# Optimization experiments

Hardware: AMD Instinct MI355X
Metric: run time of the kernel (lower is better)

## Reference

```python
import jax, jax.numpy as jnp
import numpy as np

N = 20000
E = 320000
IN = 256
H = 4
C = 64
NEG_SLOPE = 0.2


def setup_inputs() -> dict:
    key = jax.random.key(0)
    ks = jax.random.split(key, 12)
    HC = H * C

    def w(k, shape, fan_in):
        return jax.random.normal(k, shape, dtype=jnp.float32) / np.sqrt(fan_in)

    x = jax.random.normal(ks[0], (N, IN), dtype=jnp.float32)
    edge_index = jax.random.randint(ks[1], (2, E), 0, N, dtype=jnp.int64)
    return {
        "x": x,
        "edge_index": edge_index,
        "Wl1": w(ks[2], (IN, HC), IN),
        "Wr1": w(ks[3], (IN, HC), IN),
        "att1": w(ks[4], (H, C), C),
        "b1": jnp.zeros((HC,), dtype=jnp.float32),
        "Wl2": w(ks[5], (HC, HC), HC),
        "Wr2": w(ks[6], (HC, HC), HC),
        "att2": w(ks[7], (H, C), C),
        "b2": jnp.zeros((HC,), dtype=jnp.float32),
        "Wfc": w(ks[8], (HC, 2), HC),
        "bfc": jnp.zeros((2,), dtype=jnp.float32),
    }


def _gatv2(x, src, dst, Wl, Wr, att, b):
    """GATv2Conv (concat=True, share_weights=False), inference (no dropout)."""
    n = x.shape[0]
    xl = (x @ Wl).reshape(n, H, C)  # source-side projection
    xr = (x @ Wr).reshape(n, H, C)  # target-side projection
    # per-edge GATv2 score: a^T LeakyReLU(xl_j + xr_i)
    e = jax.nn.leaky_relu(xl[src] + xr[dst], NEG_SLOPE)      # [E, H, C]
    score = jnp.einsum("ehc,hc->eh", e, att)                 # [E, H]
    # segment softmax over incoming edges of each target node
    smax = jax.ops.segment_max(score, dst, num_segments=n)   # [N, H]
    ex = jnp.exp(score - smax[dst])
    denom = jax.ops.segment_sum(ex, dst, num_segments=n)     # [N, H]
    alpha = ex / denom[dst]                                  # [E, H]
    # scatter-aggregate messages (source projections weighted by alpha)
    out = jax.ops.segment_sum(alpha[:, :, None] * xl[src], dst, num_segments=n)
    return out.reshape(n, H * C) + b


def reference(x, edge_index, Wl1, Wr1, att1, b1, Wl2, Wr2, att2, b2, Wfc, bfc):
    n = x.shape[0]
    # add_self_loops=True (PyG default)
    loop = jnp.arange(n, dtype=edge_index.dtype)
    src = jnp.concatenate([edge_index[0], loop])
    dst = jnp.concatenate([edge_index[1], loop])

    h = _gatv2(x, src, dst, Wl1, Wr1, att1, b1)
    h = jax.nn.relu(h)
    h = _gatv2(h, src, dst, Wl2, Wr2, att2, b2)
    h = jax.nn.relu(h)
    g = jnp.mean(h, axis=0, keepdims=True)  # [1, H*C]
    return g @ Wfc + bfc                    # [1, 2]
```

## Files before the change

### kernel.cpp

```cpp
#include <hip/hip_runtime.h>
#include <hip/hip_bf16.h>
#include <math.h>

#define Nn 20000
#define Ee 320000
#define INF_ 256
#define Hh 4
#define Cc 64
#define HC 256
#define NEG_SLOPE 0.2f

using frag16 = __attribute__((ext_vector_type(8))) short;
using f32x4  = __attribute__((ext_vector_type(4))) float;

__device__ __forceinline__ void async16(const void* g, void* l) {
    __builtin_amdgcn_global_load_lds(
        (const __attribute__((address_space(1))) unsigned int*)g,
        (__attribute__((address_space(3))) unsigned int*)l,
        16, 0, 0);
}


__global__ void init_deg(int* deg, int n) {
    int i = blockIdx.x * blockDim.x + threadIdx.x;
    if (i < n) deg[i] = 1;
}

__global__ void hist_kernel(const int* __restrict__ dst, int ne, int* deg) {
    int e = blockIdx.x * blockDim.x + threadIdx.x;
    if (e < ne) atomicAdd(&deg[dst[e]], 1);
}

__global__ __launch_bounds__(256) void scan1(const int* __restrict__ deg,
                                             int* __restrict__ excl,
                                             int* __restrict__ bsum, int n) {
    int tid = threadIdx.x;
    int gid = blockIdx.x * 256 + tid;
    int lane = tid & 63;
    int v = (gid < n) ? deg[gid] : 0;
    int x = v;
    #pragma unroll
    for (int off = 1; off < 64; off <<= 1) {
        int y = __shfl_up(x, off, 64);
        if (lane >= off) x += y;
    }
    __shared__ int wsum[4];
    if (lane == 63) wsum[tid >> 6] = x;
    __syncthreads();
    int wadd = 0;
    for (int w = 0; w < (tid >> 6); ++w) wadd += wsum[w];
    int incl = x + wadd;
    if (gid < n) excl[gid] = incl - v;
    if (tid == 255) bsum[blockIdx.x] = incl;
}

__global__ void scan2(const int* __restrict__ bsum, int* __restrict__ boff, int nb) {
    int lane = threadIdx.x;
    int carry = 0;
    for (int base = 0; base < nb; base += 64) {
        int i = base + lane;
        int v = (i < nb) ? bsum[i] : 0;
        int x = v;
        #pragma unroll
        for (int off = 1; off < 64; off <<= 1) {
            int y = __shfl_up(x, off, 64);
            if (lane >= off) x += y;
        }
        if (i < nb) boff[i] = carry + x - v;
        carry += __shfl(x, 63, 64);
    }
    if (lane == 0) boff[nb] = carry;
}

__global__ void scan_add(int* __restrict__ row_start, int* __restrict__ cursor,
                         const int* __restrict__ boff, int n, int nb) {
    int gid = blockIdx.x * blockDim.x + threadIdx.x;
    if (gid < n) {
        int v = row_start[gid] + boff[gid >> 8];
        row_start[gid] = v;
        cursor[gid] = v;
    }
    if (gid == n) row_start[n] = boff[nb];
}

__global__ void scatter_kernel(const int* __restrict__ src, const int* __restrict__ dst,
                               int ne, int n, int* cursor, int* colx) {
    int e = blockIdx.x * blockDim.x + threadIdx.x;
    if (e < ne) {
        int d = dst[e];
        int pos = atomicAdd(&cursor[d], 1);
        colx[pos] = src[e];
    } else if (e < ne + n) {
        int node = e - ne;
        int pos = atomicAdd(&cursor[node], 1);
        colx[pos] = node;
    }
}


__device__ inline unsigned short bf16rn(float f) {
    unsigned u = __float_as_uint(f);
    unsigned r = (u + 0x7FFFu + ((u >> 16) & 1u)) >> 16;
    return (unsigned short)r;
}

__device__ inline void split1(float v, short& h, short& l) {
    unsigned short hh = bf16rn(v);
    float back = __uint_as_float(((unsigned)hh) << 16);
    unsigned short ll = bf16rn(v - back);
    h = (short)hh; l = (short)ll;
}

__device__ __forceinline__ float4 bf4_to_f4(ushort4 u) {
    return make_float4(__uint_as_float((unsigned)u.x << 16),
                       __uint_as_float((unsigned)u.y << 16),
                       __uint_as_float((unsigned)u.z << 16),
                       __uint_as_float((unsigned)u.w << 16));
}

__global__ __launch_bounds__(256) void split_kernel(const float* __restrict__ in,
                                                    short* __restrict__ hi,
                                                    short* __restrict__ lo, int n4) {
    int i = blockIdx.x * blockDim.x + threadIdx.x;
    if (i >= n4) return;
    float4 v = ((const float4*)in)[i];
    short4 h, l;
    split1(v.x, h.x, l.x);
    split1(v.y, h.y, l.y);
    split1(v.z, h.z, l.z);
    split1(v.w, h.w, l.w);
    ((short4*)hi)[i] = h;
    ((short4*)lo)[i] = l;
}

__global__ __launch_bounds__(256) void wsplit_all(const float* __restrict__ Wl1,
                                                  const float* __restrict__ Wr1,
                                                  const float* __restrict__ Wl2,
                                                  const float* __restrict__ Wr2,
                                                  short* __restrict__ WhT1,
                                                  short* __restrict__ WlT1,
                                                  short* __restrict__ WhT2,
                                                  short* __restrict__ WlT2) {
    int b = blockIdx.x;
    int n = b & 255;
    int k = threadIdx.x;
    const float* W = (b < 256) ? Wl1 : (b < 512) ? Wr1 : (b < 768) ? Wl2 : Wr2;
    short* Wh = (b < 512) ? WhT1 : WhT2;
    short* Wl = (b < 512) ? WlT1 : WlT2;
    int col = b & 511;
    float v = W[k * 256 + n];
    short h, l;
    split1(v, h, l);
    Wh[col * 256 + k] = h;
    Wl[col * 256 + k] = l;
}


__global__ __launch_bounds__(256) void mfma_gemm(const short* __restrict__ Ah,
                                                 const short* __restrict__ Al,
                                                 const short* __restrict__ WhT,
                                                 const short* __restrict__ WlT,
                                                 unsigned short* __restrict__ XLh,
                                                 float* __restrict__ XR) {
    __shared__ short BsH[64 * 256];
    __shared__ short BsL[64 * 256];

    int tid = threadIdx.x;
    int wave = tid >> 6, lane = tid & 63;
    int quad = lane >> 4, lc = lane & 15;

    int v = blockIdx.x;
    int p = (v & 7) * 157 + (v >> 3);
    int rowt = p >> 3;
    int colg = p & 7;
    int bm = rowt * 128;
    int cbase = (colg * 64) & 255;

    {
        int cl0 = wave * 2 + (lane >> 5);
        int kcs = (lane & 31) ^ (cl0 & 7);
        const short* srcH = WhT + (size_t)(colg * 64 + cl0) * HC + kcs * 8;
        const short* srcL = WlT + (size_t)(colg * 64 + cl0) * HC + kcs * 8;
        short* dstH = &BsH[wave * 512];
        short* dstL = &BsL[wave * 512];
        #pragma unroll
        for (int r = 0; r < 8; ++r) {
            async16(srcH + (size_t)r * 8 * HC, dstH + r * 2048);
            async16(srcL + (size_t)r * 8 * HC, dstL + r * 2048);
        }
    }

    int row0 = bm + wave * 32 + lc;
    int row1 = row0 + 16;
    int ca0 = (row0 < Nn) ? row0 : (Nn - 1);
    int ca1 = (row1 < Nn) ? row1 : (Nn - 1);
    const short* pa0h = Ah + (size_t)ca0 * HC + quad * 8;
    const short* pa1h = Ah + (size_t)ca1 * HC + quad * 8;
    const short* pa0l = Al + (size_t)ca0 * HC + quad * 8;
    const short* pa1l = Al + (size_t)ca1 * HC + quad * 8;

    __syncthreads();

    f32x4 acc[2][4] = {};
    #pragma unroll
    for (int c = 0; c < 8; ++c) {
        int k0 = c * 32;
        frag16 a0h = *(const frag16*)(pa0h + k0);
        frag16 a1h = *(const frag16*)(pa1h + k0);
        frag16 a0l = *(const frag16*)(pa0l + k0);
        frag16 a1l = *(const frag16*)(pa1l + k0);
        int sw = ((c * 4 + quad) ^ (lc & 7)) * 8;
        #pragma unroll
        for (int t = 0; t < 4; ++t) {
            int colL = t * 16 + lc;
            frag16 bh = *(const frag16*)&BsH[colL * HC + sw];
            frag16 bl = *(const frag16*)&BsL[colL * HC + sw];
            acc[0][t] = __builtin_amdgcn_mfma_f32_16x16x32_bf16(a0h, bh, acc[0][t], 0, 0, 0);
            acc[1][t] = __builtin_amdgcn_mfma_f32_16x16x32_bf16(a1h, bh, acc[1][t], 0, 0, 0);
            acc[0][t] = __builtin_amdgcn_mfma_f32_16x16x32_bf16(a0l, bh, acc[0][t], 0, 0, 0);
            acc[1][t] = __builtin_amdgcn_mfma_f32_16x16x32_bf16(a1l, bh, acc[1][t], 0, 0, 0);
            acc[0][t] = __builtin_amdgcn_mfma_f32_16x16x32_bf16(a0h, bl, acc[0][t], 0, 0, 0);
            acc[1][t] = __builtin_amdgcn_mfma_f32_16x16x32_bf16(a1h, bl, acc[1][t], 0, 0, 0);
        }
    }

    #pragma unroll
    for (int mt = 0; mt < 2; ++mt) {
        int rbase = bm + wave * 32 + mt * 16 + quad * 4;
        #pragma unroll
        for (int t = 0; t < 4; ++t) {
            int col = cbase + t * 16 + lc;
            #pragma unroll
            for (int r = 0; r < 4; ++r) {
                int rw = rbase + r;
                if (rw >= Nn) continue;
                if (colg < 4) XLh[(size_t)rw * HC + col] = bf16rn(acc[mt][t][r]);
                else          XR [(size_t)rw * HC + col] = acc[mt][t][r];
            }
        }
    }
}


__device__ __forceinline__ float edge_score(const float4 v, const float4 xr,
                                            const float4 a06, const float4 a04) {
    float tx = v.x + xr.x, ty = v.y + xr.y, tz = v.z + xr.z, tw = v.w + xr.w;
    float p = a06.x * tx + a04.x * fabsf(tx);
    p += a06.y * ty + a04.y * fabsf(ty);
    p += a06.z * tz + a04.z * fabsf(tz);
    p += a06.w * tw + a04.w * fabsf(tw);
    p += __shfl_xor(p, 1, 64);
    p += __shfl_xor(p, 2, 64);
    p += __shfl_xor(p, 4, 64);
    p += __shfl_xor(p, 8, 64);
    return p;
}

__global__ __launch_bounds__(256) void gat_kernel(const ushort4* __restrict__ XL4,
                                                  const float4* __restrict__ XR4,
                                                  const int* __restrict__ row_start,
                                                  const int* __restrict__ colx,
                                                  const float4* __restrict__ att4,
                                                  const float4* __restrict__ bias4,
                                                  float4* __restrict__ Hout,
                                                  short4* __restrict__ Ahi,
                                                  short4* __restrict__ Alo,
                                                  int mode) {
    int wave = threadIdx.x >> 6, lane = threadIdx.x & 63;
    int node = blockIdx.x * 4 + wave;
    float4 xr = XR4[(size_t)node * 64 + lane];
    float4 a  = att4[lane];
    float4 a06 = make_float4(a.x * 0.6f, a.y * 0.6f, a.z * 0.6f, a.w * 0.6f);
    float4 a04 = make_float4(a.x * 0.4f, a.y * 0.4f, a.z * 0.4f, a.w * 0.4f);
    int e0 = row_start[node], e1 = row_start[node + 1];
    float l0 = 0.f, l1 = 0.f;
    float4 acc0 = make_float4(0.f, 0.f, 0.f, 0.f);
    float4 acc1 = make_float4(0.f, 0.f, 0.f, 0.f);
    int e = e0;
    for (; e + 1 < e1; e += 2) {
        int s0 = __builtin_amdgcn_readfirstlane(colx[e]);
        int s1 = __builtin_amdgcn_readfirstlane(colx[e + 1]);
        ushort4 u0 = XL4[(size_t)s0 * 64 + lane];
        ushort4 u1 = XL4[(size_t)s1 * 64 + lane];
        float4 v0 = bf4_to_f4(u0);
        float4 v1 = bf4_to_f4(u1);
        float pe0 = __expf(edge_score(v0, xr, a06, a04));
        float pe1 = __expf(edge_score(v1, xr, a06, a04));
        l0 += pe0; l1 += pe1;
        acc0.x += pe0 * v0.x; acc0.y += pe0 * v0.y;
        acc0.z += pe0 * v0.z; acc0.w += pe0 * v0.w;
        acc1.x += pe1 * v1.x; acc1.y += pe1 * v1.y;
        acc1.z += pe1 * v1.z; acc1.w += pe1 * v1.w;
    }
    if (e < e1) {
        int s0 = __builtin_amdgcn_readfirstlane(colx[e]);
        float4 v0 = bf4_to_f4(XL4[(size_t)s0 * 64 + lane]);
        float pe0 = __expf(edge_score(v0, xr, a06, a04));
        l0 += pe0;
        acc0.x += pe0 * v0.x; acc0.y += pe0 * v0.y;
        acc0.z += pe0 * v0.z; acc0.w += pe0 * v0.w;
    }
    float rl = 1.f / (l0 + l1);
    float4 b = bias4[lane];
    float4 o = make_float4(fmaxf((acc0.x + acc1.x) * rl + b.x, 0.f),
                           fmaxf((acc0.y + acc1.y) * rl + b.y, 0.f),
                           fmaxf((acc0.z + acc1.z) * rl + b.z, 0.f),
                           fmaxf((acc0.w + acc1.w) * rl + b.w, 0.f));
    size_t oidx = (size_t)node * 64 + lane;
    if (mode) {
        short4 h4, l4;
        split1(o.x, h4.x, l4.x);
        split1(o.y, h4.y, l4.y);
        split1(o.z, h4.z, l4.z);
        split1(o.w, h4.w, l4.w);
        Ahi[oidx] = h4;
        Alo[oidx] = l4;
    } else {
        Hout[oidx] = o;
    }
}


__global__ void zero_f(float* p, int n) {
    int i = blockIdx.x * blockDim.x + threadIdx.x;
    if (i < n) p[i] = 0.f;
}

__global__ __launch_bounds__(256) void colsum_kernel(const float* __restrict__ Hmat,
                                                     float* __restrict__ g, int n) {
    int ch = threadIdx.x;
    float s = 0.f;
    for (int r = blockIdx.x; r < n; r += gridDim.x)
        s += Hmat[(size_t)r * HC + ch];
    atomicAdd(&g[ch], s);
}

__global__ __launch_bounds__(256) void fc_kernel(const float* __restrict__ g,
                                                 const float* __restrict__ Wfc,
                                                 const float* __restrict__ bfc,
                                                 float* __restrict__ out, float invN) {
    int t = threadIdx.x;
    float gv = g[t] * invN;
    float p0 = gv * Wfc[2 * t];
    float p1 = gv * Wfc[2 * t + 1];
    #pragma unroll
    for (int off = 32; off > 0; off >>= 1) {
        p0 += __shfl_xor(p0, off, 64);
        p1 += __shfl_xor(p1, off, 64);
    }
    __shared__ float s0[4], s1[4];
    if ((t & 63) == 0) { s0[t >> 6] = p0; s1[t >> 6] = p1; }
    __syncthreads();
    if (t == 0) {
        out[0] = s0[0] + s0[1] + s0[2] + s0[3] + bfc[0];
        out[1] = s1[0] + s1[1] + s1[2] + s1[3] + bfc[1];
    }
}


extern "C" void kernel_launch(void* const* d_in, const int* in_sizes, int n_in,
                              void* d_out, int out_size, void* d_ws, size_t ws_size,
                              hipStream_t stream) {
    const float* x    = (const float*)d_in[0];
    const int*   eidx = (const int*)d_in[1];
    const float* Wl1  = (const float*)d_in[2];
    const float* Wr1  = (const float*)d_in[3];
    const float* att1 = (const float*)d_in[4];
    const float* b1   = (const float*)d_in[5];
    const float* Wl2  = (const float*)d_in[6];
    const float* Wr2  = (const float*)d_in[7];
    const float* att2 = (const float*)d_in[8];
    const float* b2   = (const float*)d_in[9];
    const float* Wfc  = (const float*)d_in[10];
    const float* bfc  = (const float*)d_in[11];
    float* out = (float*)d_out;

    const int* srcv = eidx;
    const int* dstv = eidx + Ee;

    size_t NHC = (size_t)Nn * HC;
    float* XR = (float*)d_ws;
    float* Hb = XR + NHC;
    float* g  = Hb + NHC;
    unsigned short* XLh = (unsigned short*)(g + HC);
    short* Ah   = (short*)(XLh + NHC);
    short* Al   = Ah + NHC;
    short* WhT1 = Al + NHC;
    short* WlT1 = WhT1 + 512 * 256;
    short* WhT2 = WlT1 + 512 * 256;
    short* WlT2 = WhT2 + 512 * 256;
    int* deg       = (int*)(WlT2 + 512 * 256);
    int* row_start = deg + Nn;
    int* cursor    = row_start + (Nn + 1);
    int* colx      = cursor + Nn;
    int* bsum      = colx + (Ee + Nn);
    int* boff      = bsum + 128;

    const int NB = (Nn + 255) / 256;
    const int N4 = (int)(NHC / 4);

    init_deg<<<(Nn + 255) / 256, 256, 0, stream>>>(deg, Nn);
    hist_kernel<<<(Ee + 255) / 256, 256, 0, stream>>>(dstv, Ee, deg);
    scan1<<<NB, 256, 0, stream>>>(deg, row_start, bsum, Nn);
    scan2<<<1, 64, 0, stream>>>(bsum, boff, NB);
    scan_add<<<(Nn + 256) / 256, 256, 0, stream>>>(row_start, cursor, boff, Nn, NB);
    scatter_kernel<<<(Ee + Nn + 255) / 256, 256, 0, stream>>>(srcv, dstv, Ee, Nn, cursor, colx);

    const int GB = 157 * 8;

    wsplit_all<<<1024, 256, 0, stream>>>(Wl1, Wr1, Wl2, Wr2, WhT1, WlT1, WhT2, WlT2);
    split_kernel<<<(N4 + 255) / 256, 256, 0, stream>>>(x, Ah, Al, N4);

    mfma_gemm<<<GB, 256, 0, stream>>>(Ah, Al, WhT1, WlT1, XLh, XR);
    gat_kernel<<<Nn / 4, 256, 0, stream>>>((const ushort4*)XLh, (const float4*)XR,
                                           row_start, colx, (const float4*)att1,
                                           (const float4*)b1, (float4*)Hb,
                                           (short4*)Ah, (short4*)Al, 1);

    mfma_gemm<<<GB, 256, 0, stream>>>(Ah, Al, WhT2, WlT2, XLh, XR);
    gat_kernel<<<Nn / 4, 256, 0, stream>>>((const ushort4*)XLh, (const float4*)XR,
                                           row_start, colx, (const float4*)att2,
                                           (const float4*)b2, (float4*)Hb,
                                           (short4*)Ah, (short4*)Al, 0);

    zero_f<<<1, 256, 0, stream>>>(g, HC);
    colsum_kernel<<<256, 256, 0, stream>>>(Hb, g, Nn);
    fc_kernel<<<1, 256, 0, stream>>>(g, Wfc, bfc, out, 1.0f / Nn);
}
```

Baseline: 293.1 us.

## Swap MFMA operands for vectorized GEMM stores and prefetch edge indices

The GEMM now passes B fragments as the first MFMA operand, which transposes the accumulator layout so each lane holds four consecutive columns of one row. The epilogue can then write XL as ushort4 and XR as float4 instead of scalar stores. The loop also hoists all eight B fragment LDS reads per k-chunk and adds a launch-bounds occupancy hint. In the GAT kernel, the node's edge range is made wave-uniform and the next pair of source indices is prefetched one iteration ahead, so the index load latency is hidden behind the feature gathers.

```diff
diff --git a/kernel.cpp b/kernel.cpp
--- a/kernel.cpp
+++ b/kernel.cpp
@@ -156,12 +156,12 @@
 }
 
 
-__global__ __launch_bounds__(256) void mfma_gemm(const short* __restrict__ Ah,
-                                                 const short* __restrict__ Al,
-                                                 const short* __restrict__ WhT,
-                                                 const short* __restrict__ WlT,
-                                                 unsigned short* __restrict__ XLh,
-                                                 float* __restrict__ XR) {
+__global__ __launch_bounds__(256, 4) void mfma_gemm(const short* __restrict__ Ah,
+                                                    const short* __restrict__ Al,
+                                                    const short* __restrict__ WhT,
+                                                    const short* __restrict__ WlT,
+                                                    unsigned short* __restrict__ XLh,
+                                                    float* __restrict__ XR) {
     __shared__ short BsH[64 * 256];
     __shared__ short BsL[64 * 256];
 
@@ -210,32 +210,56 @@
         frag16 a0l = *(const frag16*)(pa0l + k0);
         frag16 a1l = *(const frag16*)(pa1l + k0);
         int sw = ((c * 4 + quad) ^ (lc & 7)) * 8;
+        frag16 bh0 = *(const frag16*)&BsH[(0 * 16 + lc) * HC + sw];
+        frag16 bh1 = *(const frag16*)&BsH[(1 * 16 + lc) * HC + sw];
+        frag16 bh2 = *(const frag16*)&BsH[(2 * 16 + lc) * HC + sw];
+        frag16 bh3 = *(const frag16*)&BsH[(3 * 16 + lc) * HC + sw];
+        frag16 bl0 = *(const frag16*)&BsL[(0 * 16 + lc) * HC + sw];
+        frag16 bl1 = *(const frag16*)&BsL[(1 * 16 + lc) * HC + sw];
+        frag16 bl2 = *(const frag16*)&BsL[(2 * 16 + lc) * HC + sw];
+        frag16 bl3 = *(const frag16*)&BsL[(3 * 16 + lc) * HC + sw];
+        acc[0][0] = __builtin_amdgcn_mfma_f32_16x16x32_bf16(bh0, a0h, acc[0][0], 0, 0, 0);
+        acc[1][0] = __builtin_amdgcn_mfma_f32_16x16x32_bf16(bh0, a1h, acc[1][0], 0, 0, 0);
+        acc[0][1] = __builtin_amdgcn_mfma_f32_16x16x32_bf16(bh1, a0h, acc[0][1], 0, 0, 0);
+        acc[1][1] = __builtin_amdgcn_mfma_f32_16x16x32_bf16(bh1, a1h, acc[1][1], 0, 0, 0);
+        acc[0][2] = __builtin_amdgcn_mfma_f32_16x16x32_bf16(bh2, a0h, acc[0][2], 0, 0, 0);
+        acc[1][2] = __builtin_amdgcn_mfma_f32_16x16x32_bf16(bh2, a1h, acc[1][2], 0, 0, 0);
+        acc[0][3] = __builtin_amdgcn_mfma_f32_16x16x32_bf16(bh3, a0h, acc[0][3], 0, 0, 0);
+        acc[1][3] = __builtin_amdgcn_mfma_f32_16x16x32_bf16(bh3, a1h, acc[1][3], 0, 0, 0);
+        acc[0][0] = __builtin_amdgcn_mfma_f32_16x16x32_bf16(bh0, a0l, acc[0][0], 0, 0, 0);
+        acc[1][0] = __builtin_amdgcn_mfma_f32_16x16x32_bf16(bh0, a1l, acc[1][0], 0, 0, 0);
+        acc[0][1] = __builtin_amdgcn_mfma_f32_16x16x32_bf16(bh1, a0l, acc[0][1], 0, 0, 0);
+        acc[1][1] = __builtin_amdgcn_mfma_f32_16x16x32_bf16(bh1, a1l, acc[1][1], 0, 0, 0);
+        acc[0][2] = __builtin_amdgcn_mfma_f32_16x16x32_bf16(bh2, a0l, acc[0][2], 0, 0, 0);
+        acc[1][2] = __builtin_amdgcn_mfma_f32_16x16x32_bf16(bh2, a1l, acc[1][2], 0, 0, 0);
+        acc[0][3] = __builtin_amdgcn_mfma_f32_16x16x32_bf16(bh3, a0l, acc[0][3], 0, 0, 0);
+        acc[1][3] = __builtin_amdgcn_mfma_f32_16x16x32_bf16(bh3, a1l, acc[1][3], 0, 0, 0);
+        acc[0][0] = __builtin_amdgcn_mfma_f32_16x16x32_bf16(bl0, a0h, acc[0][0], 0, 0, 0);
+        acc[1][0] = __builtin_amdgcn_mfma_f32_16x16x32_bf16(bl0, a1h, acc[1][0], 0, 0, 0);
+        acc[0][1] = __builtin_amdgcn_mfma_f32_16x16x32_bf16(bl1, a0h, acc[0][1], 0, 0, 0);
+        acc[1][1] = __builtin_amdgcn_mfma_f32_16x16x32_bf16(bl1, a1h, acc[1][1], 0, 0, 0);
+        acc[0][2] = __builtin_amdgcn_mfma_f32_16x16x32_bf16(bl2, a0h, acc[0][2], 0, 0, 0);
+        acc[1][2] = __builtin_amdgcn_mfma_f32_16x16x32_bf16(bl2, a1h, acc[1][2], 0, 0, 0);
+        acc[0][3] = __builtin_amdgcn_mfma_f32_16x16x32_bf16(bl3, a0h, acc[0][3], 0, 0, 0);
+        acc[1][3] = __builtin_amdgcn_mfma_f32_16x16x32_bf16(bl3, a1h, acc[1][3], 0, 0, 0);
+    }
+
+    #pragma unroll
+    for (int mt = 0; mt < 2; ++mt) {
+        int rw = bm + wave * 32 + mt * 16 + lc;
+        if (rw >= Nn) continue;
         #pragma unroll
         for (int t = 0; t < 4; ++t) {
-            int colL = t * 16 + lc;
-            frag16 bh = *(const frag16*)&BsH[colL * HC + sw];
-            frag16 bl = *(const frag16*)&BsL[colL * HC + sw];
-            acc[0][t] = __builtin_amdgcn_mfma_f32_16x16x32_bf16(a0h, bh, acc[0][t], 0, 0, 0);
-            acc[1][t] = __builtin_amdgcn_mfma_f32_16x16x32_bf16(a1h, bh, acc[1][t], 0, 0, 0);
-            acc[0][t] = __builtin_amdgcn_mfma_f32_16x16x32_bf16(a0l, bh, acc[0][t], 0, 0, 0);
-            acc[1][t] = __builtin_amdgcn_mfma_f32_16x16x32_bf16(a1l, bh, acc[1][t], 0, 0, 0);
-            acc[0][t] = __builtin_amdgcn_mfma_f32_16x16x32_bf16(a0h, bl, acc[0][t], 0, 0, 0);
-            acc[1][t] = __builtin_amdgcn_mfma_f32_16x16x32_bf16(a1h, bl, acc[1][t], 0, 0, 0);
-        }
-    }
-
-    #pragma unroll
-    for (int mt = 0; mt < 2; ++mt) {
-        int rbase = bm + wave * 32 + mt * 16 + quad * 4;
-        #pragma unroll
-        for (int t = 0; t < 4; ++t) {
-            int col = cbase + t * 16 + lc;
-            #pragma unroll
-            for (int r = 0; r < 4; ++r) {
-                int rw = rbase + r;
-                if (rw >= Nn) continue;
-                if (colg < 4) XLh[(size_t)rw * HC + col] = bf16rn(acc[mt][t][r]);
-                else          XR [(size_t)rw * HC + col] = acc[mt][t][r];
+            int col0 = cbase + t * 16 + quad * 4;
+            if (colg < 4) {
+                ushort4 o;
+                o.x = bf16rn(acc[mt][t][0]);
+                o.y = bf16rn(acc[mt][t][1]);
+                o.z = bf16rn(acc[mt][t][2]);
+                o.w = bf16rn(acc[mt][t][3]);
+                *(ushort4*)&XLh[(size_t)rw * HC + col0] = o;
+            } else {
+                *(f32x4*)&XR[(size_t)rw * HC + col0] = acc[mt][t];
             }
         }
     }
@@ -272,14 +296,21 @@
     float4 a  = att4[lane];
     float4 a06 = make_float4(a.x * 0.6f, a.y * 0.6f, a.z * 0.6f, a.w * 0.6f);
     float4 a04 = make_float4(a.x * 0.4f, a.y * 0.4f, a.z * 0.4f, a.w * 0.4f);
-    int e0 = row_start[node], e1 = row_start[node + 1];
+    int e0 = __builtin_amdgcn_readfirstlane(row_start[node]);
+    int e1 = __builtin_amdgcn_readfirstlane(row_start[node + 1]);
     float l0 = 0.f, l1 = 0.f;
     float4 acc0 = make_float4(0.f, 0.f, 0.f, 0.f);
     float4 acc1 = make_float4(0.f, 0.f, 0.f, 0.f);
+    int npairs = (e1 - e0) >> 1;
     int e = e0;
-    for (; e + 1 < e1; e += 2) {
-        int s0 = __builtin_amdgcn_readfirstlane(colx[e]);
-        int s1 = __builtin_amdgcn_readfirstlane(colx[e + 1]);
+    int s0 = 0, s1 = 0;
+    if (npairs > 0) { s0 = colx[e]; s1 = colx[e + 1]; }
+    for (int pp = 0; pp < npairs; ++pp) {
+        int en = e + 2;
+        int i0 = (en     < e1) ? en     : (e1 - 1);
+        int i1 = (en + 1 < e1) ? en + 1 : (e1 - 1);
+        int ns0 = colx[i0];
+        int ns1 = colx[i1];
         ushort4 u0 = XL4[(size_t)s0 * 64 + lane];
         ushort4 u1 = XL4[(size_t)s1 * 64 + lane];
         float4 v0 = bf4_to_f4(u0);
@@ -291,10 +322,11 @@
         acc0.z += pe0 * v0.z; acc0.w += pe0 * v0.w;
         acc1.x += pe1 * v1.x; acc1.y += pe1 * v1.y;
         acc1.z += pe1 * v1.z; acc1.w += pe1 * v1.w;
+        s0 = ns0; s1 = ns1; e = en;
     }
     if (e < e1) {
-        int s0 = __builtin_amdgcn_readfirstlane(colx[e]);
-        float4 v0 = bf4_to_f4(XL4[(size_t)s0 * 64 + lane]);
+        int st = colx[e];
+        float4 v0 = bf4_to_f4(XL4[(size_t)st * 64 + lane]);
         float pe0 = __expf(edge_score(v0, xr, a06, a04));
         l0 += pe0;
         acc0.x += pe0 * v0.x; acc0.y += pe0 * v0.y;
```

New measurement: 283.4 us. 1.03x faster.
